# Optimization experiments

Measured on AMD Instinct MI355X. Metric: run time of the kernel, lower is better.

Reference implementation:

```python
import jax, jax.numpy as jnp
import numpy as np

B, L, S, D, H, TOPK = 8, 2048, 1000, 1024, 8, 10
E = D // H  # d_keys = 128


def setup_inputs() -> dict:
    key = jax.random.key(0)
    ks = jax.random.split(key, 8)
    s = 1.0 / np.sqrt(D)
    return {
        "target_embedding": jax.random.normal(ks[0], (B, L, D), dtype=jnp.float32),
        "source_embedding": jax.random.normal(ks[1], (S, D), dtype=jnp.float32),
        "Wq": jax.random.normal(ks[2], (D, D), dtype=jnp.float32) * s,
        "bq": jnp.zeros((D,), dtype=jnp.float32),
        "Wk": jax.random.normal(ks[3], (D, D), dtype=jnp.float32) * s,
        "bk": jnp.zeros((D,), dtype=jnp.float32),
        "Wo": jax.random.normal(ks[4], (D, D), dtype=jnp.float32) * s,
        "bo": jnp.zeros((D,), dtype=jnp.float32),
        "data_id": 0,
    }


def reference(target_embedding, source_embedding, Wq, bq, Wk, bk, Wo, bo, data_id):
    # data_id is unused by the original module's math.
    b, l, d = target_embedding.shape
    h, e, topk = H, E, TOPK
    scale = 1.0 / np.sqrt(e)

    q = (target_embedding @ Wq + bq).reshape(b, l, h, e)   # [B,L,H,E]
    k = (source_embedding @ Wk + bk).reshape(-1, h, e)      # [S,H,E]

    scores = jnp.einsum('blhe,she->bhls', q, k)             # [B,H,L,S]
    A = jax.nn.softmax(scale * scores, axis=-1)             # dropout is eval-mode identity
    tmps = A.sum(axis=2)                                    # [B,H,S] head-wise column mass
    _, idxs = jax.lax.top_k(tmps, topk)                     # [B,H,topk]

    kh = jnp.transpose(k, (1, 0, 2))                        # [H,S,E]
    # gather per (batch, head) the topk source key vectors
    tok = kh[jnp.arange(h)[None, :, None], idxs, :]         # [B,H,topk,E]
    tok = jnp.transpose(tok, (0, 2, 1, 3)).reshape(b, topk, h * e)  # [B,topk,D]
    return tok @ Wo + bo                                    # [B,topk,D]
```

## Files before the change

kernel.cpp:

```cpp
#include <hip/hip_runtime.h>
#include <hip/hip_bf16.h>
#include <math.h>

constexpr int B_ = 8;
constexpr int L_ = 2048;
constexpr int S_ = 1000;
constexpr int D_ = 1024;
constexpr int H_ = 8;
constexpr int E_ = 128;
constexpr int TOPK_ = 10;
constexpr float SCALE_LOG2E_ = 0.12751744f;

typedef __attribute__((ext_vector_type(8))) short short8;
typedef __attribute__((ext_vector_type(4))) float f32x4;

__device__ inline unsigned short f2bf(float x) {
    unsigned u = __float_as_uint(x);
    unsigned r = (u + 0x7fffu + ((u >> 16) & 1u)) >> 16;
    return (unsigned short)r;
}
__device__ inline float bf2f(unsigned short s) {
    return __uint_as_float(((unsigned)s) << 16);
}

__device__ __forceinline__ float fexp2(float x) {
#if __has_builtin(__builtin_amdgcn_exp2f)
    return __builtin_amdgcn_exp2f(x);
#else
    return __expf(x * 0.69314718056f);
#endif
}

typedef __attribute__((address_space(1))) const unsigned int gas_u32;
typedef __attribute__((address_space(3))) unsigned int las_u32;
__device__ __forceinline__ void gload_lds16(const void* g, void* l) {
    __builtin_amdgcn_global_load_lds((gas_u32*)g, (las_u32*)l, 16, 0, 0);
}

__global__ __launch_bounds__(256) void gemm_bias_kernel(
    const float* __restrict__ A, const float* __restrict__ Bm,
    const float* __restrict__ bias, float* __restrict__ C,
    int M, int N, int Kd)
{
    __shared__ float As[16][65];
    __shared__ float Bs[16][68];

    const int t  = threadIdx.x;
    const int tx = t & 15;
    const int ty = t >> 4;
    const int m0 = blockIdx.y * 64;
    const int n0 = blockIdx.x * 64;

    float acc[4][4];
#pragma unroll
    for (int i = 0; i < 4; ++i)
#pragma unroll
        for (int j = 0; j < 4; ++j) acc[i][j] = 0.f;

    for (int k0 = 0; k0 < Kd; k0 += 16) {
        {
            const int row = t >> 2;
            const int c4  = (t & 3) * 4;
            float4 v = {0.f, 0.f, 0.f, 0.f};
            if (m0 + row < M)
                v = *(const float4*)&A[(size_t)(m0 + row) * Kd + k0 + c4];
            As[c4 + 0][row] = v.x;
            As[c4 + 1][row] = v.y;
            As[c4 + 2][row] = v.z;
            As[c4 + 3][row] = v.w;
        }
        {
            const int row = t >> 4;
            const int c4  = (t & 15) * 4;
            float4 v = *(const float4*)&Bm[(size_t)(k0 + row) * N + n0 + c4];
            *(float4*)&Bs[row][c4] = v;
        }
        __syncthreads();
#pragma unroll
        for (int k = 0; k < 16; ++k) {
            float a[4], b[4];
#pragma unroll
            for (int i = 0; i < 4; ++i) a[i] = As[k][ty * 4 + i];
            float4 bv = *(const float4*)&Bs[k][tx * 4];
            b[0] = bv.x; b[1] = bv.y; b[2] = bv.z; b[3] = bv.w;
#pragma unroll
            for (int i = 0; i < 4; ++i)
#pragma unroll
                for (int j = 0; j < 4; ++j) acc[i][j] += a[i] * b[j];
        }
        __syncthreads();
    }

#pragma unroll
    for (int i = 0; i < 4; ++i) {
        const int row = m0 + ty * 4 + i;
        if (row < M) {
#pragma unroll
            for (int j = 0; j < 4; ++j) {
                const int col = n0 + tx * 4 + j;
                C[(size_t)row * N + col] = acc[i][j] + bias[col];
            }
        }
    }
}

__global__ __launch_bounds__(256) void splitWT_kernel(
    const float* __restrict__ W,
    unsigned short* __restrict__ WTh, unsigned short* __restrict__ WTl)
{
    __shared__ __attribute__((aligned(16))) float tile[64][68];
    const int t  = threadIdx.x;
    const int k0 = blockIdx.y * 64, n0 = blockIdx.x * 64;
#pragma unroll
    for (int it = 0; it < 4; ++it) {
        int id = it * 256 + t;
        int r = id >> 4, c = id & 15;
        *(float4*)&tile[r][c * 4] = *(const float4*)&W[(size_t)(k0 + r) * D_ + n0 + c * 4];
    }
    __syncthreads();
#pragma unroll
    for (int it = 0; it < 4; ++it) {
        int id = it * 256 + t;
        int n = id >> 4, c = id & 15;
        unsigned short hs[4], ls[4];
#pragma unroll
        for (int i = 0; i < 4; ++i) {
            float x = tile[c * 4 + i][n];
            hs[i] = f2bf(x);
            ls[i] = f2bf(x - bf2f(hs[i]));
        }
        size_t o = (size_t)(n0 + n) * D_ + k0 + c * 4;
        uint2 uh; uh.x = (unsigned)hs[0] | ((unsigned)hs[1] << 16);
                  uh.y = (unsigned)hs[2] | ((unsigned)hs[3] << 16);
        uint2 ul; ul.x = (unsigned)ls[0] | ((unsigned)ls[1] << 16);
                  ul.y = (unsigned)ls[2] | ((unsigned)ls[3] << 16);
        *(uint2*)&WTh[o] = uh;
        *(uint2*)&WTl[o] = ul;
    }
}

__global__ __launch_bounds__(256) void split_src_kernel(
    const float* __restrict__ src,
    unsigned short* __restrict__ Sh, unsigned short* __restrict__ Sl)
{
    int idx  = blockIdx.x * 256 + threadIdx.x;
    int base = idx * 4;
    int row  = base >> 10;
    float4 v = {0.f, 0.f, 0.f, 0.f};
    if (row < S_) v = *(const float4*)&src[base];
    float xs[4] = {v.x, v.y, v.z, v.w};
    unsigned short hs[4], ls[4];
#pragma unroll
    for (int i = 0; i < 4; ++i) {
        hs[i] = f2bf(xs[i]);
        ls[i] = f2bf(xs[i] - bf2f(hs[i]));
    }
    uint2 uh; uh.x = (unsigned)hs[0] | ((unsigned)hs[1] << 16);
              uh.y = (unsigned)hs[2] | ((unsigned)hs[3] << 16);
    uint2 ul; ul.x = (unsigned)ls[0] | ((unsigned)ls[1] << 16);
              ul.y = (unsigned)ls[2] | ((unsigned)ls[3] << 16);
    *(uint2*)&Sh[base] = uh;
    *(uint2*)&Sl[base] = ul;
}

__global__ __launch_bounds__(256, 2) void kproj_kernel(
    const unsigned short* __restrict__ Sh, const unsigned short* __restrict__ Sl,
    const unsigned short* __restrict__ WkTh, const unsigned short* __restrict__ WkTl,
    const float* __restrict__ bk,
    float* __restrict__ Kbuf,
    unsigned short* __restrict__ Kh, unsigned short* __restrict__ Kl)
{
    __shared__ __attribute__((aligned(16))) unsigned short Ah[128 * 64];
    __shared__ __attribute__((aligned(16))) unsigned short Al[128 * 64];
    __shared__ __attribute__((aligned(16))) unsigned short Bh[128 * 64];
    __shared__ __attribute__((aligned(16))) unsigned short Bl[128 * 64];

    const int t    = threadIdx.x;
    const int lane = t & 63, w = t >> 6;
    const int mb   = blockIdx.x >> 3;
    const int n0   = (blockIdx.x & 7) * 128;

    f32x4 acc[2][8];
#pragma unroll
    for (int m = 0; m < 2; ++m)
#pragma unroll
        for (int n = 0; n < 8; ++n) acc[m][n] = (f32x4){0.f, 0.f, 0.f, 0.f};

    for (int k0 = 0; k0 < D_; k0 += 64) {
        __syncthreads();
#pragma unroll
        for (int it = 0; it < 4; ++it) {
            int r = it * 32 + (t >> 3), c = t & 7;
            size_t gofs = (size_t)r * D_ + k0 + ((c ^ (r & 7)) << 3);
            int db = it * 4096 + t * 16;
            gload_lds16(&Sh[(size_t)(mb * 128) * D_ + gofs], (char*)Ah + db);
            gload_lds16(&Sl[(size_t)(mb * 128) * D_ + gofs], (char*)Al + db);
            gload_lds16(&WkTh[(size_t)n0 * D_ + gofs], (char*)Bh + db);
            gload_lds16(&WkTl[(size_t)n0 * D_ + gofs], (char*)Bl + db);
        }
        __syncthreads();

#pragma unroll
        for (int ki = 0; ki < 2; ++ki) {
            short8 ah[2], al[2];
#pragma unroll
            for (int m = 0; m < 2; ++m) {
                int r = w * 32 + m * 16 + (lane & 15);
                int slot = ki * 4 + (lane >> 4);
                int lofs = r * 64 + ((slot ^ (r & 7)) << 3);
                ah[m] = *(short8*)&Ah[lofs];
                al[m] = *(short8*)&Al[lofs];
            }
#pragma unroll
            for (int n = 0; n < 8; ++n) {
                int nn = n * 16 + (lane & 15);
                int slot = ki * 4 + (lane >> 4);
                int lofs = nn * 64 + ((slot ^ (nn & 7)) << 3);
                short8 bh = *(short8*)&Bh[lofs];
                short8 bl = *(short8*)&Bl[lofs];
#pragma unroll
                for (int m = 0; m < 2; ++m) {
                    acc[m][n] = __builtin_amdgcn_mfma_f32_16x16x32_bf16(ah[m], bh, acc[m][n], 0, 0, 0);
                    acc[m][n] = __builtin_amdgcn_mfma_f32_16x16x32_bf16(ah[m], bl, acc[m][n], 0, 0, 0);
                    acc[m][n] = __builtin_amdgcn_mfma_f32_16x16x32_bf16(al[m], bh, acc[m][n], 0, 0, 0);
                }
            }
        }
    }

#pragma unroll
    for (int n = 0; n < 8; ++n) {
        int col = n0 + n * 16 + (lane & 15);
        float bkv = bk[col];
#pragma unroll
        for (int m = 0; m < 2; ++m) {
            int rbase = mb * 128 + w * 32 + m * 16 + ((lane >> 4) << 2);
#pragma unroll
            for (int r = 0; r < 4; ++r) {
                int row = rbase + r;
                unsigned short hh = 0, ll = 0;
                if (row < S_) {
                    float kv = acc[m][n][r] + bkv;
                    Kbuf[(size_t)row * D_ + col] = kv;
                    hh = f2bf(kv);
                    ll = f2bf(kv - bf2f(hh));
                }
                Kh[(size_t)row * D_ + col] = hh;
                Kl[(size_t)row * D_ + col] = ll;
            }
        }
    }
}

__global__ __launch_bounds__(256, 2) void qproj_kernel(
    const float* __restrict__ tgt,
    const unsigned short* __restrict__ WqTh, const unsigned short* __restrict__ WqTl,
    const float* __restrict__ bq,
    unsigned short* __restrict__ qhb, unsigned short* __restrict__ qlb)
{
    __shared__ __attribute__((aligned(16))) float          Af[2][128 * 32];
    __shared__ __attribute__((aligned(16))) unsigned short Bh[2][128 * 32];
    __shared__ __attribute__((aligned(16))) unsigned short Bl[2][128 * 32];

    const int t    = threadIdx.x;
    const int lane = t & 63, w = t >> 6;
    const int mb   = blockIdx.x >> 3;
    const int n0   = (blockIdx.x & 7) * 128;

    f32x4 acc[2][8];
#pragma unroll
    for (int m = 0; m < 2; ++m)
#pragma unroll
        for (int n = 0; n < 8; ++n) acc[m][n] = (f32x4){0.f, 0.f, 0.f, 0.f};

#define QP_ISSUE(KT, BUF)                                                   \
    do {                                                                    \
        _Pragma("unroll")                                                   \
        for (int it = 0; it < 4; ++it) {          \
            int id = it * 256 + t;                                          \
            int r = id >> 3, c = id & 7;          \
            size_t ga = (size_t)(mb * 128 + r) * D_ + (KT) * 32             \
                        + ((c ^ (r & 7)) << 2);                             \
            gload_lds16(&tgt[ga], (char*)&Af[(BUF)][0] + it * 4096 + t * 16); \
        }                                                                   \
        _Pragma("unroll")                                                   \
        for (int it = 0; it < 2; ++it) {      \
            int id = it * 256 + t;                                          \
            int r = id >> 2, c = id & 3;         \
            size_t gb = (size_t)(n0 + r) * D_ + (KT) * 32                   \
                        + ((c ^ (r & 3)) << 3);                             \
            int db = it * 4096 + t * 16;                                    \
            gload_lds16(&WqTh[gb], (char*)&Bh[(BUF)][0] + db);              \
            gload_lds16(&WqTl[gb], (char*)&Bl[(BUF)][0] + db);              \
        }                                                                   \
    } while (0)

    QP_ISSUE(0, 0);
    int cur = 0;
    for (int kt = 0; kt < 32; ++kt) {
        __syncthreads();
        if (kt < 31) QP_ISSUE(kt + 1, cur ^ 1);

        short8 ah[2], al[2];
#pragma unroll
        for (int m = 0; m < 2; ++m) {
            int r  = w * 32 + m * 16 + (lane & 15);
            int c0 = (lane >> 4) * 2;
            float4 x0 = *(float4*)&Af[cur][r * 32 + ((c0 ^ (r & 7)) << 2)];
            float4 x1 = *(float4*)&Af[cur][r * 32 + (((c0 + 1) ^ (r & 7)) << 2)];
            float xs[8] = {x0.x, x0.y, x0.z, x0.w, x1.x, x1.y, x1.z, x1.w};
#pragma unroll
            for (int j = 0; j < 8; ++j) {
                unsigned short hh = f2bf(xs[j]);
                ah[m][j] = (short)hh;
                al[m][j] = (short)f2bf(xs[j] - bf2f(hh));
            }
        }
#pragma unroll
        for (int n = 0; n < 8; ++n) {
            int nn = n * 16 + (lane & 15);
            int lofs = nn * 32 + (((lane >> 4) ^ (nn & 3)) << 3);
            short8 bh = *(short8*)&Bh[cur][lofs];
            short8 bl = *(short8*)&Bl[cur][lofs];
#pragma unroll
            for (int m = 0; m < 2; ++m) {
                acc[m][n] = __builtin_amdgcn_mfma_f32_16x16x32_bf16(ah[m], bh, acc[m][n], 0, 0, 0);
                acc[m][n] = __builtin_amdgcn_mfma_f32_16x16x32_bf16(ah[m], bl, acc[m][n], 0, 0, 0);
                acc[m][n] = __builtin_amdgcn_mfma_f32_16x16x32_bf16(al[m], bh, acc[m][n], 0, 0, 0);
            }
        }
        cur ^= 1;
    }
#undef QP_ISSUE

#pragma unroll
    for (int n = 0; n < 8; ++n) {
        int col = n0 + n * 16 + (lane & 15);
        float bqv = bq[col];
#pragma unroll
        for (int m = 0; m < 2; ++m) {
            int rbase = mb * 128 + w * 32 + m * 16 + ((lane >> 4) << 2);
#pragma unroll
            for (int r = 0; r < 4; ++r) {
                float q = (acc[m][n][r] + bqv) * SCALE_LOG2E_;
                unsigned short hh = f2bf(q);
                qhb[(size_t)(rbase + r) * D_ + col] = hh;
                qlb[(size_t)(rbase + r) * D_ + col] = f2bf(q - bf2f(hh));
            }
        }
    }
}

__global__ __launch_bounds__(256, 2) void scores2p_kernel(
    const unsigned short* __restrict__ qhb, const unsigned short* __restrict__ qlb,
    const unsigned short* __restrict__ Kh, const unsigned short* __restrict__ Kl,
    float* __restrict__ tmps, int b0)
{
    __shared__ __attribute__((aligned(16))) unsigned short SH[2][32 * 128];
    __shared__ __attribute__((aligned(16))) unsigned short SL[2][32 * 128];
    __shared__ float tmps_l[1024];

    const int t    = threadIdx.x;
    const int lane = t & 63, w = t >> 6;
    const int blk  = blockIdx.x;
    const int bb   = blk >> 6;
    const int h    = (blk >> 3) & 7;
    const int lt   = blk & 7;
    const int qrow0 = bb * L_ + lt * 256;
    const int bh_i  = (b0 + bb) * H_ + h;
    const int kr0   = t >> 4;
    const int kc0   = t & 15;

    for (int i = t; i < 1024; i += 256) tmps_l[i] = 0.f;

#define SC_ISSUE0(ST, BUF)                                                  \
    do {                                                                    \
        _Pragma("unroll")                                                   \
        for (int it = 0; it < 4; ++it) {                                    \
            int r = it * 16 + kr0;                                          \
            size_t g = (size_t)((ST) * 64 + r) * D_ + h * E_                \
                       + ((kc0 ^ (r & 15)) << 3);                           \
            char* base = (it < 2) ? (char*)&SH[(BUF)][0]                    \
                                  : (char*)&SL[(BUF)][0];                   \
            int db = (it & 1) * 4096 + t * 16;                              \
            gload_lds16(&Kh[g], base + db);                                 \
        }                                                                   \
    } while (0)

#define SC_ISSUE2(ST, BUF)                                                  \
    do {                                                                    \
        _Pragma("unroll")                                                   \
        for (int it = 0; it < 2; ++it) {                                    \
            int r = it * 16 + kr0;                                          \
            size_t g = (size_t)((ST) * 32 + r) * D_ + h * E_                \
                       + ((kc0 ^ (r & 15)) << 3);                           \
            int db = it * 4096 + t * 16;                                    \
            gload_lds16(&Kh[g], (char*)&SH[(BUF)][0] + db);                 \
            gload_lds16(&Kl[g], (char*)&SL[(BUF)][0] + db);                 \
        }                                                                   \
    } while (0)

    SC_ISSUE0(0, 1);

    short8 qh[4][4], ql[4][4];
#pragma unroll
    for (int ch = 0; ch < 8; ++ch) {
        __syncthreads();
#pragma unroll
        for (int it = 0; it < 2; ++it) {
            int r = it * 16 + kr0;
            size_t g = (size_t)(qrow0 + ch * 32 + r) * D_ + h * E_ + kc0 * 8;
            int lofs = r * 128 + ((kc0 ^ (r & 15)) << 3);
            *(uint4*)&SH[0][lofs] = *(const uint4*)&qhb[g];
            *(uint4*)&SL[0][lofs] = *(const uint4*)&qlb[g];
        }
        __syncthreads();
        if ((ch >> 1) == w) {
#pragma unroll
            for (int j = 0; j < 2; ++j) {
                int rg = (ch & 1) * 2 + j;
#pragma unroll
                for (int ki = 0; ki < 4; ++ki) {
                    int rq = j * 16 + (lane & 15);
                    int slot = ki * 4 + (lane >> 4);
                    int lofs = rq * 128 + ((slot ^ (rq & 15)) << 3);
                    qh[rg][ki] = *(short8*)&SH[0][lofs];
                    ql[rg][ki] = *(short8*)&SL[0][lofs];
                }
            }
        }
    }

    float zacc[4][4];
#pragma unroll
    for (int rg = 0; rg < 4; ++rg)
#pragma unroll
        for (int r = 0; r < 4; ++r) zacc[rg][r] = 0.f;
    float invZ[4][4];

    int cur = 1;

    for (int u = 0; u < 16; ++u) {
        __syncthreads();
        if (u < 15) SC_ISSUE0(u + 1, cur ^ 1);
        else        SC_ISSUE2(0, cur ^ 1);

#pragma unroll
        for (int nfh = 0; nfh < 2; ++nfh) {
            f32x4 acc[4][2];
#pragma unroll
            for (int rg = 0; rg < 4; ++rg)
#pragma unroll
                for (int n2 = 0; n2 < 2; ++n2) acc[rg][n2] = (f32x4){0.f, 0.f, 0.f, 0.f};

#pragma unroll
            for (int ki = 0; ki < 4; ++ki)
#pragma unroll
                for (int n2 = 0; n2 < 2; ++n2) {
                    int nf = nfh * 2 + n2;
                    int sr = nf * 16 + (lane & 15);
                    int slot = ki * 4 + (lane >> 4);
                    int lofs = (sr & 31) * 128 + ((slot ^ (sr & 15)) << 3);
                    short8 bh = (nf < 2) ? *(short8*)&SH[cur][lofs]
                                         : *(short8*)&SL[cur][lofs];
#pragma unroll
                    for (int rg = 0; rg < 4; ++rg)
                        acc[rg][n2] = __builtin_amdgcn_mfma_f32_16x16x32_bf16(qh[rg][ki], bh, acc[rg][n2], 0, 0, 0);
                }

#pragma unroll
            for (int n2 = 0; n2 < 2; ++n2) {
                int s = u * 64 + (nfh * 2 + n2) * 16 + (lane & 15);
                if (s < S_) {
#pragma unroll
                    for (int rg = 0; rg < 4; ++rg)
#pragma unroll
                        for (int r = 0; r < 4; ++r)
                            zacc[rg][r] += fexp2(acc[rg][n2][r]);
                }
            }
        }

        if (u == 15) {
#pragma unroll
            for (int rg = 0; rg < 4; ++rg)
#pragma unroll
                for (int r = 0; r < 4; ++r) {
                    float z = zacc[rg][r];
                    z += __shfl_xor(z, 1);
                    z += __shfl_xor(z, 2);
                    z += __shfl_xor(z, 4);
                    z += __shfl_xor(z, 8);
                    invZ[rg][r] = 1.f / z;
                }
        }
        cur ^= 1;
    }

    for (int u = 0; u < 32; ++u) {
        __syncthreads();
        if (u < 31) SC_ISSUE2(u + 1, cur ^ 1);

        f32x4 acc[4][2];
#pragma unroll
        for (int rg = 0; rg < 4; ++rg)
#pragma unroll
            for (int nf = 0; nf < 2; ++nf) acc[rg][nf] = (f32x4){0.f, 0.f, 0.f, 0.f};

#pragma unroll
        for (int ki = 0; ki < 4; ++ki)
#pragma unroll
            for (int nf = 0; nf < 2; ++nf) {
                int sr = nf * 16 + (lane & 15);
                int slot = ki * 4 + (lane >> 4);
                int lofs = sr * 128 + ((slot ^ (sr & 15)) << 3);
                short8 bh = *(short8*)&SH[cur][lofs];
                short8 bl = *(short8*)&SL[cur][lofs];
#pragma unroll
                for (int rg = 0; rg < 4; ++rg) {
                    acc[rg][nf] = __builtin_amdgcn_mfma_f32_16x16x32_bf16(qh[rg][ki], bh, acc[rg][nf], 0, 0, 0);
                    acc[rg][nf] = __builtin_amdgcn_mfma_f32_16x16x32_bf16(qh[rg][ki], bl, acc[rg][nf], 0, 0, 0);
                    acc[rg][nf] = __builtin_amdgcn_mfma_f32_16x16x32_bf16(ql[rg][ki], bh, acc[rg][nf], 0, 0, 0);
                }
            }

#pragma unroll
        for (int nf = 0; nf < 2; ++nf) {
            int s = u * 32 + nf * 16 + (lane & 15);
            if (s < S_) {
                float val = 0.f;
#pragma unroll
                for (int rg = 0; rg < 4; ++rg)
#pragma unroll
                    for (int r = 0; r < 4; ++r)
                        val += fexp2(acc[rg][nf][r]) * invZ[rg][r];
                atomicAdd(&tmps_l[s], val);
            }
        }
        cur ^= 1;
    }
#undef SC_ISSUE0
#undef SC_ISSUE2

    __syncthreads();
    for (int i = t; i < S_; i += 256)
        atomicAdd(&tmps[(size_t)bh_i * S_ + i], tmps_l[i]);
}

__global__ __launch_bounds__(256) void topk_kernel(
    const float* __restrict__ tmps, int* __restrict__ idxs)
{
    const int bh = blockIdx.x;
    const int t  = threadIdx.x;
    __shared__ float v[S_];
    __shared__ float rv[256];
    __shared__ int   ri[256];

    for (int i = t; i < S_; i += 256) v[i] = tmps[(size_t)bh * S_ + i];
    __syncthreads();

    for (int it = 0; it < TOPK_; ++it) {
        float best = -1e38f;
        int bi = 0x7fffffff;
        for (int s = t; s < S_; s += 256) {
            const float x = v[s];
            if (x > best) { best = x; bi = s; }
        }
        rv[t] = best; ri[t] = bi;
        __syncthreads();
        for (int k = 128; k > 0; k >>= 1) {
            if (t < k) {
                const float x = rv[t + k];
                const int  xi = ri[t + k];
                if (x > rv[t] || (x == rv[t] && xi < ri[t])) { rv[t] = x; ri[t] = xi; }
            }
            __syncthreads();
        }
        if (t == 0) {
            idxs[bh * TOPK_ + it] = ri[0];
            v[ri[0]] = -1e38f;
        }
        __syncthreads();
    }
}

__global__ __launch_bounds__(256) void gather_kernel(
    const float* __restrict__ K, const int* __restrict__ idxs,
    float* __restrict__ tok)
{
    const int o = blockIdx.x * 256 + threadIdx.x;
    if (o >= B_ * TOPK_ * D_) return;
    const int d  = o & (D_ - 1);
    const int tt = (o >> 10) % TOPK_;
    const int b  = o / (D_ * TOPK_);
    const int h  = d >> 7;
    const int s  = idxs[(b * H_ + h) * TOPK_ + tt];
    tok[o] = K[(size_t)s * D_ + d];
}

extern "C" void kernel_launch(void* const* d_in, const int* in_sizes, int n_in,
                              void* d_out, int out_size, void* d_ws, size_t ws_size,
                              hipStream_t stream)
{
    const float* tgt = (const float*)d_in[0];
    const float* src = (const float*)d_in[1];
    const float* Wq  = (const float*)d_in[2];
    const float* bq  = (const float*)d_in[3];
    const float* Wk  = (const float*)d_in[4];
    const float* bk  = (const float*)d_in[5];
    const float* Wo  = (const float*)d_in[6];
    const float* bo  = (const float*)d_in[7];
    float* out = (float*)d_out;

    char* ws = (char*)d_ws;
    size_t off = 0;
    float*          Kbuf = (float*)(ws + off);          off += (size_t)S_ * D_ * 4;
    float*          tmps = (float*)(ws + off);          off += (size_t)B_ * H_ * S_ * 4;
    int*            idxs = (int*)(ws + off);            off += (size_t)B_ * H_ * TOPK_ * 4;
    off = (off + 255) & ~(size_t)255;
    float*          tok  = (float*)(ws + off);          off += (size_t)B_ * TOPK_ * D_ * 4;
    unsigned short* Kh   = (unsigned short*)(ws + off); off += (size_t)1024 * D_ * 2;
    unsigned short* Kl   = (unsigned short*)(ws + off); off += (size_t)1024 * D_ * 2;
    unsigned short* WqTh = (unsigned short*)(ws + off); off += (size_t)D_ * D_ * 2;
    unsigned short* WqTl = (unsigned short*)(ws + off); off += (size_t)D_ * D_ * 2;
    unsigned short* WkTh = (unsigned short*)(ws + off); off += (size_t)D_ * D_ * 2;
    unsigned short* WkTl = (unsigned short*)(ws + off); off += (size_t)D_ * D_ * 2;
    unsigned short* Sh   = (unsigned short*)(ws + off); off += (size_t)1024 * D_ * 2;
    unsigned short* Sl   = (unsigned short*)(ws + off); off += (size_t)1024 * D_ * 2;
    unsigned short* planes = (unsigned short*)(ws + off);
    const size_t fixed_bytes = off;
    const size_t plane_elems_per_b = (size_t)L_ * D_;

    int nb_fit = 1;
    if (ws_size > fixed_bytes) {
        size_t f = (ws_size - fixed_bytes) / (2 * plane_elems_per_b * 2);
        nb_fit = (f < 1) ? 1 : (f > 8 ? 8 : (int)f);
    }

    hipMemsetAsync(tmps, 0, (size_t)B_ * H_ * S_ * sizeof(float), stream);

    split_src_kernel<<<(1024 * D_) / (256 * 4), 256, 0, stream>>>(src, Sh, Sl);
    {
        dim3 g(D_ / 64, D_ / 64);
        splitWT_kernel<<<g, 256, 0, stream>>>(Wq, WqTh, WqTl);
        splitWT_kernel<<<g, 256, 0, stream>>>(Wk, WkTh, WkTl);
    }

    kproj_kernel<<<64, 256, 0, stream>>>(Sh, Sl, WkTh, WkTl, bk, Kbuf, Kh, Kl);

    for (int b0 = 0; b0 < B_; b0 += nb_fit) {
        int nb = (B_ - b0 < nb_fit) ? (B_ - b0) : nb_fit;
        unsigned short* qhb = planes;
        unsigned short* qlb = qhb + (size_t)nb_fit * plane_elems_per_b;

        qproj_kernel<<<nb * 128, 256, 0, stream>>>(
            tgt + (size_t)b0 * L_ * D_, WqTh, WqTl, bq, qhb, qlb);
        scores2p_kernel<<<nb * 64, 256, 0, stream>>>(qhb, qlb, Kh, Kl, tmps, b0);
    }

    topk_kernel<<<B_ * H_, 256, 0, stream>>>(tmps, idxs);
    gather_kernel<<<(B_ * TOPK_ * D_ + 255) / 256, 256, 0, stream>>>(Kbuf, idxs, tok);
    {
        dim3 g(D_ / 64, (B_ * TOPK_ + 63) / 64);
        gemm_bias_kernel<<<g, 256, 0, stream>>>(tok, Wo, bo, out, B_ * TOPK_, D_, D_);
    }
}
```

Before: 404.9 us.

## Swizzle qproj LDS layout over 256-byte lines and remap block order

Changes the Q-projection kernel's shared-memory layout so that XOR swizzling spans 16 sixteen-byte slots (256-byte lines of two A rows or four B rows) instead of per-row swizzles, to reduce LDS bank conflicts on the fragment reads. It also remaps blockIdx so that consecutive blocks share the same N tile across different M blocks, which is meant to improve L2 reuse of the weight tiles. Index math becomes more complex and the global-load coalescing pattern changes.

```diff
diff --git a/kernel.cpp b/kernel.cpp
--- a/kernel.cpp
+++ b/kernel.cpp
@@ -264,8 +264,10 @@
 
     const int t    = threadIdx.x;
     const int lane = t & 63, w = t >> 6;
-    const int mb   = blockIdx.x >> 3;
-    const int n0   = (blockIdx.x & 7) * 128;
+    const int x    = blockIdx.x & 7;
+    const int jj   = blockIdx.x >> 3;
+    const int n0   = (jj & 7) * 128;
+    const int mb   = (jj >> 3) * 8 + x;
 
     f32x4 acc[2][8];
 #pragma unroll
@@ -276,22 +278,23 @@
 #define QP_ISSUE(KT, BUF)                                                   \
     do {                                                                    \
         _Pragma("unroll")                                                   \
-        for (int it = 0; it < 4; ++it) {          \
+        for (int it = 0; it < 4; ++it) {                       \
             int id = it * 256 + t;                                          \
-            int r = id >> 3, c = id & 7;          \
-            size_t ga = (size_t)(mb * 128 + r) * D_ + (KT) * 32             \
-                        + ((c ^ (r & 7)) << 2);                             \
-            gload_lds16(&tgt[ga], (char*)&Af[(BUF)][0] + it * 4096 + t * 16); \
+            int line = id >> 4, sub = id & 15;                              \
+            int gs = sub ^ (line & 15);                                     \
+            size_t ga = (size_t)(mb * 128 + line * 2 + (gs >> 3)) * D_      \
+                        + (KT) * 32 + ((gs & 7) << 2);                      \
+            gload_lds16(&tgt[ga], (char*)&Af[(BUF)][0] + id * 16);          \
         }                                                                   \
         _Pragma("unroll")                                                   \
-        for (int it = 0; it < 2; ++it) {      \
+        for (int it = 0; it < 2; ++it) {                      \
             int id = it * 256 + t;                                          \
-            int r = id >> 2, c = id & 3;         \
-            size_t gb = (size_t)(n0 + r) * D_ + (KT) * 32                   \
-                        + ((c ^ (r & 3)) << 3);                             \
-            int db = it * 4096 + t * 16;                                    \
-            gload_lds16(&WqTh[gb], (char*)&Bh[(BUF)][0] + db);              \
-            gload_lds16(&WqTl[gb], (char*)&Bl[(BUF)][0] + db);              \
+            int line = id >> 4, sub = id & 15;                              \
+            int gs = sub ^ (line & 15);                                     \
+            size_t gb = (size_t)(n0 + line * 4 + (gs >> 2)) * D_            \
+                        + (KT) * 32 + ((gs & 3) << 3);                      \
+            gload_lds16(&WqTh[gb], (char*)&Bh[(BUF)][0] + id * 16);         \
+            gload_lds16(&WqTl[gb], (char*)&Bl[(BUF)][0] + id * 16);         \
         }                                                                   \
     } while (0)
 
@@ -304,22 +307,26 @@
         short8 ah[2], al[2];
 #pragma unroll
         for (int m = 0; m < 2; ++m) {
-            int r  = w * 32 + m * 16 + (lane & 15);
-            int c0 = (lane >> 4) * 2;
-            float4 x0 = *(float4*)&Af[cur][r * 32 + ((c0 ^ (r & 7)) << 2)];
-            float4 x1 = *(float4*)&Af[cur][r * 32 + (((c0 + 1) ^ (r & 7)) << 2)];
+            int r    = w * 32 + m * 16 + (lane & 15);
+            int c0   = (lane >> 4) * 2;
+            int line = r >> 1;
+            int sub0 = (r & 1) * 8 + c0;
+            float4 x0 = *(float4*)&Af[cur][line * 64 + ((sub0 ^ (line & 15)) << 2)];
+            float4 x1 = *(float4*)&Af[cur][line * 64 + (((sub0 + 1) ^ (line & 15)) << 2)];
             float xs[8] = {x0.x, x0.y, x0.z, x0.w, x1.x, x1.y, x1.z, x1.w};
 #pragma unroll
-            for (int j = 0; j < 8; ++j) {
-                unsigned short hh = f2bf(xs[j]);
-                ah[m][j] = (short)hh;
-                al[m][j] = (short)f2bf(xs[j] - bf2f(hh));
+            for (int jjj = 0; jjj < 8; ++jjj) {
+                unsigned short hh = f2bf(xs[jjj]);
+                ah[m][jjj] = (short)hh;
+                al[m][jjj] = (short)f2bf(xs[jjj] - bf2f(hh));
             }
         }
 #pragma unroll
         for (int n = 0; n < 8; ++n) {
-            int nn = n * 16 + (lane & 15);
-            int lofs = nn * 32 + (((lane >> 4) ^ (nn & 3)) << 3);
+            int nn   = n * 16 + (lane & 15);
+            int line = nn >> 2;
+            int sub  = (nn & 3) * 4 + (lane >> 4);
+            int lofs = line * 128 + ((sub ^ (line & 15)) << 3);
             short8 bh = *(short8*)&Bh[cur][lofs];
             short8 bl = *(short8*)&Bl[cur][lofs];
 #pragma unroll
```

New measurement: 381.9 us, median of 2. 1.06x faster.
